# Kernel tuning notes

Hardware: AMD Instinct MI355X
Metric: run time of the kernel (lower is better)

The kernel has to match this reference:

```python
import jax, jax.numpy as jnp
import numpy as np

K = 3; STRIDE = 1; PAD = 1
IN_C = 256; OUT_C = 512
M = 5; TABLE_SIZE = 16
D = K * K * IN_C  # 2304


def _P(v, m):
    # ALSH preprocessing transform: append norm powers ||v||^2, ||v||^4, ...
    n2 = jnp.sum(v * v)
    powers = jnp.stack([n2 ** (2 ** i) for i in range(m)])
    return jnp.concatenate([v, powers])


def _Q(v, m):
    # ALSH query transform: append m halves
    return jnp.concatenate([v, jnp.full((m,), 0.5, v.dtype)])


def _hash_index(a, v):
    # hf followed by fmod(table_size).abs() as in the torch module
    h = jnp.floor(jnp.dot(a, v))
    return jnp.abs(jnp.mod(h, TABLE_SIZE)).astype(jnp.int32)


def _im2col(x):
    # x: (N, C, H, W) -> (K*K*C, N*h2*w2), rows ordered (kh, kw, c) to match
    # the (out, k, k, in) kernel flattening of the original module.
    N, C, H, W = x.shape
    h2 = (H - K + 2 * PAD) // STRIDE + 1
    w2 = (W - K + 2 * PAD) // STRIDE + 1
    xp = jnp.pad(x, ((0, 0), (0, 0), (PAD, PAD), (PAD, PAD)))
    cols = []
    for i in range(K):          # small fixed loop (k*k = 9)
        for j in range(K):
            cols.append(xp[:, :, i:i + h2 * STRIDE:STRIDE, j:j + w2 * STRIDE:STRIDE])
    p = jnp.stack(cols, 0)                 # (K*K, N, C, h2, w2)
    p = p.transpose(0, 2, 1, 3, 4)         # (K*K, C, N, h2, w2)
    return p.reshape(K * K * C, N * h2 * w2), h2, w2


def setup_inputs() -> dict:
    key = jax.random.key(0)
    k1, k2, k3, k4 = jax.random.split(key, 4)
    stdv = 1.0 / np.sqrt(IN_C * K * K)
    x = jax.random.normal(k1, (16, IN_C, 56, 56), dtype=jnp.float32)
    kernels = jax.random.uniform(k2, (OUT_C, D), dtype=jnp.float32,
                                 minval=-stdv, maxval=stdv)
    bias = jax.random.uniform(k3, (1, OUT_C, 1, 1), dtype=jnp.float32,
                              minval=-stdv, maxval=stdv)
    a = jax.random.normal(k4, (D + M,), dtype=jnp.float32)
    return {"x": x, "kernels": kernels, "bias": bias, "a": a, "mode": 0}


def reference(x, kernels, bias, a, mode):
    N = x.shape[0]
    patch_matr, h2, w2 = _im2col(x)  # (D, N*h2*w2)

    # --- build ALSH table: hash index per kernel row (non-differentiable) ---
    kernel_idx = jax.lax.stop_gradient(
        jax.vmap(lambda kr: _hash_index(a, _P(kr, M)))(kernels))  # (OUT_C,)

    # --- query: max over each patch row, normalized to unit vector ---
    max_row = patch_matr.max(axis=1)                    # (D,)
    unit = max_row / jnp.linalg.norm(max_row)
    q_idx = jax.lax.stop_gradient(_hash_index(a, _Q(unit, M)))

    # --- routed subset matmul, expressed as a row mask (jit-safe) ---
    mask = (kernel_idx == q_idx)                        # (OUT_C,) bool
    count = mask.sum()
    full = kernels @ patch_matr                         # (OUT_C, N*h2*w2)
    scale = jnp.where(count > 0, count / OUT_C, 1.0).astype(full.dtype)
    out = jnp.where(count > 0,
                    jnp.where(mask[:, None], full, 0.0) / scale,
                    full)

    out = out.reshape(OUT_C, N, h2 * w2).transpose(1, 0, 2)
    out = out.reshape(N, OUT_C, h2, w2)
    return out + bias
```

## Files before the change

kernel.cpp:

```cpp
#include <hip/hip_runtime.h>
#include <math.h>

#define IN_C   256
#define OUT_C  512
#define HW     3136
#define W_     56
#define D_     2304
#define TBL    16


#define XB_OFF 2375680ULL
#define XB_ROW 1856
#define P_OFF  7483392

typedef __attribute__((ext_vector_type(8))) __bf16 bf16x8;
typedef __attribute__((ext_vector_type(4))) float f32x4;

__device__ __forceinline__ ushort f2bf(float f) {
  uint b = __float_as_uint(f);
  b = b + 0x7FFFu + ((b >> 16) & 1u);
  return (ushort)(b >> 16);
}


__global__ __launch_bounds__(256) void k_setup(const float* __restrict__ x,
                                               const float* __restrict__ kern,
                                               const float* __restrict__ a,
                                               float* __restrict__ ws) {
  __shared__ __align__(16) float smem[64 * 57];
  int bx = blockIdx.x, t = threadIdx.x;

  if (bx < 3712) {
    int c0i = bx & 3;
    int n = (bx >> 2) & 15;
    int yp = bx >> 6;
    int c0 = c0i * 64, cgbase = c0i * 2;
    ushort* xb = (ushort*)((char*)ws + XB_OFF);
    const size_t CGS = (size_t)16 * 58 * XB_ROW;
    size_t rb0 = (size_t)(n * 58 + yp) * XB_ROW;
    uint4 z4 = make_uint4(0u, 0u, 0u, 0u);

    if (yp == 0 || yp == 57) {
      for (int e = t; e < 464; e += 256) {
        int cg_l = e / 232, k = e - cg_l * 232;
        *(uint4*)&xb[rb0 + (size_t)(cgbase + cg_l) * CGS + (size_t)k * 8] = z4;
      }
      return;
    }
    if (t < 16) {
      int cg_l = t >> 3, r = t & 7;
      int wp = (r >> 2) ? 57 : 0, oct = r & 3;
      *(uint4*)&xb[rb0 + (size_t)(cgbase + cg_l) * CGS + wp * 32 + oct * 8] = z4;
    }
    int y = yp - 1;
    float* Lf = smem;
    for (int e = t; e < 3584; e += 256) {
      int ci = e / 56, w = e - ci * 56;
      Lf[ci * 57 + w] = x[(size_t)(n * 256 + c0 + ci) * 3136 + y * 56 + w];
    }
    __syncthreads();
    for (int e = t; e < 448; e += 256) {
      int w = e >> 3, cg_l = (e >> 2) & 1, oct = e & 3;
      int cb = cg_l * 32 + oct * 8;
      uint pk[4];
#pragma unroll
      for (int k = 0; k < 4; k++) {
        uint lo = f2bf(Lf[(cb + 2 * k) * 57 + w]);
        uint hi = f2bf(Lf[(cb + 2 * k + 1) * 57 + w]);
        pk[k] = lo | (hi << 16);
      }
      *(uint4*)&xb[rb0 + (size_t)(cgbase + cg_l) * CGS + (w + 1) * 32 + oct * 8] =
          make_uint4(pk[0], pk[1], pk[2], pk[3]);
    }
  } else if (bx < 4736) {
    int idx = bx - 3712;
    int c = idx & 255, part = idx >> 8;
    float m[3][3];
#pragma unroll
    for (int i = 0; i < 3; i++)
#pragma unroll
      for (int j = 0; j < 3; j++) m[i][j] = -INFINITY;
    for (int e = t; e < 4 * HW; e += 256) {
      int nl = e / HW;
      int rem = e - nl * HW;
      int r = rem / W_;
      int s = rem - r * W_;
      float v = x[(size_t)((part * 4 + nl) * IN_C + c) * HW + rem];
      bool rc[3] = { r <= 54, true, r >= 1 };
      bool sc[3] = { s <= 54, true, s >= 1 };
#pragma unroll
      for (int i = 0; i < 3; i++)
#pragma unroll
        for (int j = 0; j < 3; j++)
          if (rc[i] && sc[j]) m[i][j] = fmaxf(m[i][j], v);
    }
#pragma unroll
    for (int i = 0; i < 3; i++)
#pragma unroll
      for (int j = 0; j < 3; j++)
        for (int o = 32; o; o >>= 1)
          m[i][j] = fmaxf(m[i][j], __shfl_down(m[i][j], o, 64));
    float* red = smem;
    int lane = t & 63, wid = t >> 6;
    if (lane == 0) {
#pragma unroll
      for (int i = 0; i < 3; i++)
#pragma unroll
        for (int j = 0; j < 3; j++) red[wid * 9 + i * 3 + j] = m[i][j];
    }
    __syncthreads();
    if (t < 9) {
      float v = fmaxf(fmaxf(red[0 * 9 + t], red[1 * 9 + t]),
                      fmaxf(red[2 * 9 + t], red[3 * 9 + t]));
      ws[P_OFF + (size_t)part * 2304 + (size_t)t * IN_C + c] = v;
    }
  } else if (bx < 5248) {
    int o = bx - 4736;
    const float* kr = kern + (size_t)o * D_;
    double sd = 0, sn = 0;
    for (int d = t; d < D_; d += 256) {
      double w = (double)kr[d];
      sd += (double)a[d] * w;
      sn += w * w;
    }
    double* sh = (double*)smem;
    double* sh2 = sh + 8;
    int lane = t & 63, wid = t >> 6;
    for (int off = 32; off; off >>= 1) {
      sd += __shfl_down(sd, off, 64);
      sn += __shfl_down(sn, off, 64);
    }
    if (lane == 0) { sh[wid] = sd; sh2[wid] = sn; }
    __syncthreads();
    if (t == 0) {
      double td = 0, tn = 0;
      for (int w = 0; w < 4; w++) { td += sh[w]; tn += sh2[w]; }
      double p1 = tn, p2 = p1 * p1, p4 = p2 * p2, p8 = p4 * p4, p16 = p8 * p8;
      td += (double)a[D_] * p1 + (double)a[D_ + 1] * p2 + (double)a[D_ + 2] * p4 +
            (double)a[D_ + 3] * p8 + (double)a[D_ + 4] * p16;
      long long h = (long long)floor(td);
      ((int*)ws)[2304 + o] = (int)((h % TBL + TBL) % TBL);
    }
  } else {
    int s = bx - 5248;
    uint* Wc = (uint*)((char*)ws + 16384);
    const float* src = kern + (size_t)s * D_;
    for (int e = t; e < 1152; e += 256) {
      uint lo = f2bf(src[2 * e]);
      uint hi = f2bf(src[2 * e + 1]);
      Wc[(size_t)s * 1152 + e] = lo | (hi << 16);
    }
  }
}

__global__ __launch_bounds__(512) void k_route(const float* __restrict__ a,
                                               float* __restrict__ ws) {
  int t = threadIdx.x;
  const float* P = ws + P_OFF;
  __shared__ double sh[8], sh2[8];
  __shared__ int shq, c1, c2;
  double sd = 0.0, sq = 0.0;
  if (t < 256) {
    for (int d = t; d < D_; d += 256) {
      float v = fmaxf(fmaxf(P[d], P[2304 + d]), fmaxf(P[4608 + d], P[6912 + d]));
      if ((d >> 8) != 4) v = fmaxf(v, 0.0f);
      double dv = (double)v;
      sd += (double)a[d] * dv;
      sq += dv * dv;
    }
    for (int o = 32; o; o >>= 1) {
      sd += __shfl_down(sd, o, 64);
      sq += __shfl_down(sq, o, 64);
    }
    if ((t & 63) == 0) { sh[t >> 6] = sd; sh2[t >> 6] = sq; }
  }
  __syncthreads();
  if (t == 0) {
    double td = 0, tq = 0;
    for (int w = 0; w < 4; w++) { td += sh[w]; tq += sh2[w]; }
    double dot = td / sqrt(tq);
    dot += 0.5 * ((double)a[D_] + (double)a[D_ + 1] + (double)a[D_ + 2] +
                  (double)a[D_ + 3] + (double)a[D_ + 4]);
    long long h = (long long)floor(dot);
    int q = (int)((h % TBL + TBL) % TBL);
    ((int*)ws)[2816] = q;
    shq = q;
    c1 = 0; c2 = 0;
  }
  __syncthreads();
  int* hashk = (int*)ws + 2304;
  int* cntp = (int*)ws + 2817;
  float* scalep = ws + 2818;
  int* active = (int*)ws + 2819;
  int* inact = (int*)ws + 3331;
  int q = shq;
  bool m = (hashk[t] == q);
  if (m) active[atomicAdd(&c1, 1)] = t;
  else   inact[atomicAdd(&c2, 1)] = t;
  __syncthreads();
  int c = c1;
  if (c == 0) active[t] = t;
  if (t == 0) {
    if (c > 0) { *cntp = c; *scalep = 512.0f / (float)c; }
    else       { *cntp = 512; *scalep = 1.0f; }
  }
}

#define XSTR 40
#define XSTRIDE 40
#define ASTRIDE 104

__global__ __launch_bounds__(256, 1) void k_convx(const float* __restrict__ bias,
                                                  const float* __restrict__ ws,
                                                  float* __restrict__ out) {
  const int* iws = (const int*)ws;
  int cnt = iws[2817];
  int octile = blockIdx.y;
  int rt = blockIdx.x;
  int n = blockIdx.z;
  int t = threadIdx.x;

  {
    int base = octile * 128;
    int lo = base < cnt ? cnt : base;
    int hi = base + 128;
    if (lo < hi) {
      const int* inact = iws + 3331;
      size_t nbase = (size_t)n * OUT_C * HW;
      int nin = hi - lo;
      for (int e = t; e < nin * 112; e += 256) {
        int j = e / 112, f = e - j * 112;
        int oc = inact[lo - cnt + j];
        float bv = bias[oc];
        ((float4*)out)[(nbase + (size_t)oc * HW) / 4 + rt * 112 + f] =
            make_float4(bv, bv, bv, bv);
      }
    }
    if (base >= cnt) return;
  }

  float sc = ws[2818];
  const int* active = iws + 2819;
  const char* Wcb = (const char*)ws + 16384;
  const ushort* xb = (const ushort*)((const char*)ws + XB_OFF);

  int lane = t & 63, wid = t >> 6;
  int quad = lane >> 4, l16 = lane & 15;

  __shared__ __align__(16) ushort X_lds[2][580 * XSTR];
  __shared__ __align__(16) ushort A_lds[2][128 * XSTR];

  int pbase[7];
#pragma unroll
  for (int b = 0; b < 7; b++) {
    int pxl = wid * 112 + b * 16 + l16;
    int rl = pxl / 56;
    int col = pxl - rl * 56;
    pbase[b] = ((rl + 1) * 58 + (col + 1)) * XSTR;
  }

  int r0 = t >> 2;
  int slot0 = octile * 128 + r0;
  int slot1 = slot0 + 64;
  int aoc0 = (slot0 < cnt) ? active[slot0] : 0;
  int aoc1 = (slot1 < cnt) ? active[slot1] : 0;
  const char* Wr0 = Wcb + (size_t)aoc0 * 4608 + (t & 3) * 16;
  const char* Wr1 = Wcb + (size_t)aoc1 * 4608 + (t & 3) * 16;
  int aoff0 = r0 * XSTR + (t & 3) * 8;
  int aoff1 = (r0 + 64) * XSTR + (t & 3) * 8;

  const size_t CGS = (size_t)16 * 58 * XB_ROW;
  const ushort* xsrc = xb + (size_t)(n * 58 + rt * 8) * XB_ROW;

  f32x4 acc[8][7];
#pragma unroll
  for (int a = 0; a < 8; a++)
#pragma unroll
    for (int b = 0; b < 7; b++) acc[a][b] = (f32x4){0.f, 0.f, 0.f, 0.f};

  uint4 xh0 = {}, xh1 = {};

  {
    uint4 a0 = *(const uint4*)Wr0;
    uint4 a1 = *(const uint4*)Wr1;
    *(uint4*)&A_lds[0][aoff0] = a0;
    *(uint4*)&A_lds[0][aoff1] = a1;
    for (int j = t; j < 2320; j += 256)
      *(uint4*)&X_lds[0][(j >> 2) * XSTR + (j & 3) * 8] =
          *(const uint4*)(xsrc + (size_t)j * 8);
  }
  __syncthreads();

  for (int cc = 0; cc < 8; ++cc) {
    const int xc = cc & 1;
#pragma unroll
    for (int tap = 0; tap < 9; ++tap) {
      const int cur = (cc + tap) & 1;
      const int tapn = (tap + 1) % 9;
      const int ccn = cc + (tap + 1) / 9;
      const bool havenext = !(cc == 7 && tap == 8);
      uint4 na0, na1;
      if (havenext) {
        int off = tapn * 512 + ccn * 64;
        na0 = *(const uint4*)(Wr0 + off);
        na1 = *(const uint4*)(Wr1 + off);
      }
      const bool xi = (tap < 8) && (cc < 7);
      uint4 xv0, xv1;
      if (xi) {
        int xj = tap * 290 + t;
        xv0 = *(const uint4*)(xsrc + (size_t)(cc + 1) * CGS + (size_t)xj * 8);
        if (t < 34)
          xv1 = *(const uint4*)(xsrc + (size_t)(cc + 1) * CGS +
                                (size_t)(xj + 256) * 8);
      }

      const int kh = tap / 3, kw = tap - kh * 3;
      const int poff = ((kh - 1) * 58 + (kw - 1)) * XSTR + quad * 8;
      bf16x8 xf[7];
#pragma unroll
      for (int b = 0; b < 7; b++) {
        union { uint4 u; bf16x8 v; } cv;
        cv.u = *(const uint4*)&X_lds[xc][pbase[b] + poff];
        xf[b] = cv.v;
      }
      __builtin_amdgcn_s_setprio(1);
#pragma unroll
      for (int a = 0; a < 8; a++) {
        union { uint4 u; bf16x8 v; } av;
        av.u = *(const uint4*)&A_lds[cur][(a * 16 + l16) * XSTR + quad * 8];
        bf16x8 af = av.v;
#pragma unroll
        for (int b = 0; b < 7; b++)
          acc[a][b] = __builtin_amdgcn_mfma_f32_16x16x32_bf16(af, xf[b],
                                                              acc[a][b], 0, 0, 0);
      }
      __builtin_amdgcn_s_setprio(0);

      if (havenext) {
        *(uint4*)&A_lds[cur ^ 1][aoff0] = na0;
        *(uint4*)&A_lds[cur ^ 1][aoff1] = na1;
      }
      if (tap >= 1 && cc < 7) {
        int hj = (tap - 1) * 290 + t;
        *(uint4*)&X_lds[xc ^ 1][(hj >> 2) * XSTR + (hj & 3) * 8] = xh0;
        if (t < 34) {
          int hj2 = hj + 256;
          *(uint4*)&X_lds[xc ^ 1][(hj2 >> 2) * XSTR + (hj2 & 3) * 8] = xh1;
        }
      }
      xh0 = xv0; xh1 = xv1;
      __syncthreads();
    }
  }

  size_t nbase = (size_t)n * OUT_C * HW;
#pragma unroll
  for (int a = 0; a < 8; a++) {
#pragma unroll
    for (int r = 0; r < 4; r++) {
      int slot = octile * 128 + a * 16 + quad * 4 + r;
      if (slot < cnt) {
        int oc = active[slot];
        float bv = bias[oc];
        size_t obase = nbase + (size_t)oc * HW + rt * 448 + wid * 112 + l16;
#pragma unroll
        for (int b = 0; b < 7; b++)
          out[obase + b * 16] = acc[a][b][r] * sc + bv;
      }
    }
  }
}


__global__ __launch_bounds__(256) void k_chanmax(const float* __restrict__ x,
                                                 float* __restrict__ ws) {
  int c = blockIdx.x, t = threadIdx.x;
  float m[3][3];
#pragma unroll
  for (int i = 0; i < 3; i++)
#pragma unroll
    for (int j = 0; j < 3; j++) m[i][j] = -INFINITY;
  for (int e = t; e < 16 * HW; e += 256) {
    int n = e / HW;
    int rem = e - n * HW;
    int r = rem / W_;
    int s = rem - r * W_;
    float v = x[(size_t)(n * IN_C + c) * HW + rem];
    bool rc[3] = { r <= 54, true, r >= 1 };
    bool sc[3] = { s <= 54, true, s >= 1 };
#pragma unroll
    for (int i = 0; i < 3; i++)
#pragma unroll
      for (int j = 0; j < 3; j++)
        if (rc[i] && sc[j]) m[i][j] = fmaxf(m[i][j], v);
  }
#pragma unroll
  for (int i = 0; i < 3; i++)
#pragma unroll
    for (int j = 0; j < 3; j++)
      for (int o = 32; o; o >>= 1)
        m[i][j] = fmaxf(m[i][j], __shfl_down(m[i][j], o, 64));
  __shared__ float red[4][9];
  int lane = t & 63, wid = t >> 6;
  if (lane == 0) {
#pragma unroll
    for (int i = 0; i < 3; i++)
#pragma unroll
      for (int j = 0; j < 3; j++) red[wid][i * 3 + j] = m[i][j];
  }
  __syncthreads();
  if (t < 9) {
    float v = fmaxf(fmaxf(red[0][t], red[1][t]), fmaxf(red[2][t], red[3][t]));
    int i = t / 3, j = t - i * 3;
    if (i != 1 || j != 1) v = fmaxf(v, 0.0f);
    ws[(size_t)t * IN_C + c] = v;
  }
}

__global__ __launch_bounds__(256) void k_qhash(const float* __restrict__ a,
                                               float* __restrict__ ws) {
  const float* max_row = ws;
  int t = threadIdx.x;
  double sd = 0.0, sq = 0.0;
  for (int d = t; d < D_; d += 256) {
    double v = (double)max_row[d];
    sd += (double)a[d] * v;
    sq += v * v;
  }
  __shared__ double sh[8], sh2[8];
  int lane = t & 63, wid = t >> 6;
  for (int o = 32; o; o >>= 1) {
    sd += __shfl_down(sd, o, 64);
    sq += __shfl_down(sq, o, 64);
  }
  if (lane == 0) { sh[wid] = sd; sh2[wid] = sq; }
  __syncthreads();
  if (t == 0) {
    double td = 0, tq = 0;
    for (int w = 0; w < 4; w++) { td += sh[w]; tq += sh2[w]; }
    double dot = td / sqrt(tq);
    dot += 0.5 * ((double)a[D_] + (double)a[D_ + 1] + (double)a[D_ + 2] +
                  (double)a[D_ + 3] + (double)a[D_ + 4]);
    long long h = (long long)floor(dot);
    ((int*)ws)[2816] = (int)((h % TBL + TBL) % TBL);
  }
}

__global__ __launch_bounds__(256) void k_khash(const float* __restrict__ kern,
                                               const float* __restrict__ a,
                                               float* __restrict__ ws) {
  int o = blockIdx.x, t = threadIdx.x;
  const float* kr = kern + (size_t)o * D_;
  double sd = 0, sn = 0;
  for (int d = t; d < D_; d += 256) {
    double w = (double)kr[d];
    sd += (double)a[d] * w;
    sn += w * w;
  }
  __shared__ double sh[8], sh2[8];
  int lane = t & 63, wid = t >> 6;
  for (int off = 32; off; off >>= 1) {
    sd += __shfl_down(sd, off, 64);
    sn += __shfl_down(sn, off, 64);
  }
  if (lane == 0) { sh[wid] = sd; sh2[wid] = sn; }
  __syncthreads();
  if (t == 0) {
    double td = 0, tn = 0;
    for (int w = 0; w < 4; w++) { td += sh[w]; tn += sh2[w]; }
    double p1 = tn, p2 = p1 * p1, p4 = p2 * p2, p8 = p4 * p4, p16 = p8 * p8;
    td += (double)a[D_] * p1 + (double)a[D_ + 1] * p2 + (double)a[D_ + 2] * p4 +
          (double)a[D_ + 3] * p8 + (double)a[D_ + 4] * p16;
    long long h = (long long)floor(td);
    ((int*)ws)[2304 + o] = (int)((h % TBL + TBL) % TBL);
  }
}

__global__ __launch_bounds__(512) void k_select(float* __restrict__ ws) {
  int t = threadIdx.x;
  int* hashk = (int*)ws + 2304;
  int* qidx = (int*)ws + 2816;
  int* cntp = (int*)ws + 2817;
  float* scalep = ws + 2818;
  int* active = (int*)ws + 2819;
  int* flags = (int*)ws + 3331;
  __shared__ int cnt;
  if (t == 0) cnt = 0;
  active[t] = 0;
  __syncthreads();
  int q = *qidx;
  bool m = (hashk[t] == q);
  if (m) {
    int p = atomicAdd(&cnt, 1);
    active[p] = t;
  }
  __syncthreads();
  int c = cnt;
  flags[t] = (c == 0) ? 1 : (m ? 1 : 0);
  if (c == 0) active[t] = t;
  if (t == 0) {
    if (c > 0) { *cntp = c; *scalep = 512.0f / (float)c; }
    else       { *cntp = 512; *scalep = 1.0f; }
  }
}

__global__ __launch_bounds__(256) void k_prep(const float* __restrict__ kern,
                                              float* __restrict__ ws) {
  const int* iws = (const int*)ws;
  int cnt = iws[2817];
  const int* active = iws + 2819;
  ushort* Wc = (ushort*)((char*)ws + 16384);
  int s = blockIdx.x, t = threadIdx.x;
  if (s < cnt) {
    int oc = active[s];
    const float* src = kern + (size_t)oc * D_;
    for (int e = t; e < D_; e += 256) Wc[(size_t)s * D_ + e] = f2bf(src[e]);
  } else {
    for (int e = t; e < D_; e += 256) Wc[(size_t)s * D_ + e] = 0;
  }
}

__global__ __launch_bounds__(256) void k_biasfill(const float* __restrict__ bias,
                                                  const float* __restrict__ ws,
                                                  float* __restrict__ out) {
  const int* flags = (const int*)ws + 3331;
  const int total4 = 16 * OUT_C * HW / 4;
  int stride = gridDim.x * blockDim.x;
  for (int i = blockIdx.x * blockDim.x + threadIdx.x; i < total4; i += stride) {
    int o = (i / 784) & (OUT_C - 1);
    if (!flags[o]) {
      float b = bias[o];
      ((float4*)out)[i] = make_float4(b, b, b, b);
    }
  }
}

__global__ __launch_bounds__(256, 2) void k_conv(const float* __restrict__ x,
                                                 const float* __restrict__ bias,
                                                 const float* __restrict__ ws,
                                                 float* __restrict__ out) {
  const int* iws = (const int*)ws;
  int cnt = iws[2817];
  int octile = blockIdx.y;
  if (octile * 128 >= cnt) return;
  float sc = ws[2818];
  const int* active = iws + 2819;
  const ushort* Wc = (const ushort*)((const char*)ws + 16384);
  int rt = blockIdx.x;
  int n = blockIdx.z;
  int t = threadIdx.x;
  int lane = t & 63, wid = t >> 6;
  int quad = lane >> 4, l16 = lane & 15;
  int ochalf = wid & 1, pxhalf = wid >> 1;
  __shared__ __align__(16) ushort X_lds[348 * XSTRIDE];
  __shared__ __align__(16) ushort A_lds[128 * ASTRIDE];
  const float* xin = x + (size_t)n * IN_C * HW;
  int pbase[7];
#pragma unroll
  for (int b = 0; b < 7; b++) {
    int pxl = pxhalf * 112 + b * 16 + l16;
    int rl = pxl / 56;
    int col = pxl - rl * 56;
    pbase[b] = ((rl + 1) * 58 + (col + 1)) * XSTRIDE;
  }
  f32x4 acc[4][7];
#pragma unroll
  for (int a = 0; a < 4; a++)
#pragma unroll
    for (int b = 0; b < 7; b++) acc[a][b] = (f32x4){0.f, 0.f, 0.f, 0.f};
  for (int cc = 0; cc < 8; ++cc) {
    int c0 = cc * 32;
    __syncthreads();
    for (int e = t; e < 1392; e += 256) {
      int q = e / 348;
      int p = e - q * 348;
      int rl = p / 58;
      int cp = p - rl * 58;
      int y = rt * 4 - 1 + rl;
      int xx = cp - 1;
      float vv[8];
      if ((unsigned)y < 56u && (unsigned)xx < 56u) {
        const float* src = xin + (size_t)(c0 + q * 8) * HW + y * W_ + xx;
#pragma unroll
        for (int k = 0; k < 8; k++) vv[k] = src[(size_t)k * HW];
      } else {
#pragma unroll
        for (int k = 0; k < 8; k++) vv[k] = 0.f;
      }
      uint4 pk;
      pk.x = (uint)f2bf(vv[0]) | ((uint)f2bf(vv[1]) << 16);
      pk.y = (uint)f2bf(vv[2]) | ((uint)f2bf(vv[3]) << 16);
      pk.z = (uint)f2bf(vv[4]) | ((uint)f2bf(vv[5]) << 16);
      pk.w = (uint)f2bf(vv[6]) | ((uint)f2bf(vv[7]) << 16);
      *(uint4*)&X_lds[p * XSTRIDE + q * 8] = pk;
    }
    for (int kh = 0; kh < 3; ++kh) {
      __syncthreads();
      for (int e = t; e < 1536; e += 256) {
        int oc = e / 12;
        int seg = e - oc * 12;
        int tl = seg >> 2, q = seg & 3;
        uint4 v = *(const uint4*)(Wc + (size_t)(octile * 128 + oc) * D_ +
                                  (kh * 3 + tl) * IN_C + c0 + q * 8);
        *(uint4*)&A_lds[oc * ASTRIDE + tl * 32 + q * 8] = v;
      }
      __syncthreads();
      int di = kh - 1;
#pragma unroll
      for (int djj = 0; djj < 3; ++djj) {
        int poff = (di * 58 + (djj - 1)) * XSTRIDE + quad * 8;
        bf16x8 bfr[7];
#pragma unroll
        for (int b = 0; b < 7; b++) {
          union { uint4 u; bf16x8 v; } cv;
          cv.u = *(const uint4*)&X_lds[pbase[b] + poff];
          bfr[b] = cv.v;
        }
#pragma unroll
        for (int a = 0; a < 4; a++) {
          union { uint4 u; bf16x8 v; } cv;
          cv.u = *(const uint4*)&A_lds[(ochalf * 64 + a * 16 + l16) * ASTRIDE +
                                       djj * 32 + quad * 8];
          bf16x8 af = cv.v;
#pragma unroll
          for (int b = 0; b < 7; b++)
            acc[a][b] = __builtin_amdgcn_mfma_f32_16x16x32_bf16(af, bfr[b],
                                                                acc[a][b], 0, 0, 0);
        }
      }
    }
  }
  size_t nbase = (size_t)n * OUT_C * HW;
#pragma unroll
  for (int a = 0; a < 4; a++) {
#pragma unroll
    for (int r = 0; r < 4; r++) {
      int slot = octile * 128 + ochalf * 64 + a * 16 + quad * 4 + r;
      if (slot < cnt) {
        int oc = active[slot];
        float bv = bias[oc];
        size_t obase = nbase + (size_t)oc * HW + rt * 224 + pxhalf * 112 + l16;
#pragma unroll
        for (int b = 0; b < 7; b++)
          out[obase + b * 16] = acc[a][b][r] * sc + bv;
      }
    }
  }
}

extern "C" void kernel_launch(void* const* d_in, const int* in_sizes, int n_in,
                              void* d_out, int out_size, void* d_ws, size_t ws_size,
                              hipStream_t stream) {
  const float* x    = (const float*)d_in[0];
  const float* kern = (const float*)d_in[1];
  const float* bias = (const float*)d_in[2];
  const float* a    = (const float*)d_in[3];
  float* out = (float*)d_out;
  float* ws  = (float*)d_ws;

  const size_t need = 29933568ULL + 4 * 2304 * 4;

  if (ws_size >= need) {
    k_setup<<<dim3(5760), dim3(256), 0, stream>>>(x, kern, a, ws);
    k_route<<<dim3(1), dim3(512), 0, stream>>>(a, ws);
    k_convx<<<dim3(7, 4, 16), dim3(256), 0, stream>>>(bias, ws, out);
  } else {
    k_chanmax<<<dim3(IN_C), dim3(256), 0, stream>>>(x, ws);
    k_qhash<<<dim3(1), dim3(256), 0, stream>>>(a, ws);
    k_khash<<<dim3(OUT_C), dim3(256), 0, stream>>>(kern, a, ws);
    k_select<<<dim3(1), dim3(512), 0, stream>>>(ws);
    k_prep<<<dim3(OUT_C), dim3(256), 0, stream>>>(kern, ws);
    k_biasfill<<<dim3(4096), dim3(256), 0, stream>>>(bias, ws, out);
    k_conv<<<dim3(14, 4, 16), dim3(256), 0, stream>>>(x, bias, ws, out);
  }
}
```

Before: 323.0 us.

## Double output-channel tile per block to 256 with 512-thread blocks sharing X tile

The conv kernel now uses 512-thread blocks covering 256 output channels, where before it used 256 threads and 128 channels. Two wave groups split the channel range and share one staged input-patch tile in LDS. This halves the number of blocks and the redundant X loads across channel tiles, and spreads X staging over more threads. The costs are a larger LDS footprint, fewer blocks (224) on a large-CU GPU, and more idle work when few channels are active, since whole 256-channel tiles compute even when the count is small.

```diff
diff --git a/kernel.cpp b/kernel.cpp
--- a/kernel.cpp
+++ b/kernel.cpp
@@ -210,7 +210,7 @@
 #define XSTRIDE 40
 #define ASTRIDE 104
 
-__global__ __launch_bounds__(256, 1) void k_convx(const float* __restrict__ bias,
+__global__ __launch_bounds__(512, 2) void k_convx(const float* __restrict__ bias,
                                                   const float* __restrict__ ws,
                                                   float* __restrict__ out) {
   const int* iws = (const int*)ws;
@@ -221,14 +221,14 @@
   int t = threadIdx.x;
 
   {
-    int base = octile * 128;
+    int base = octile * 256;
     int lo = base < cnt ? cnt : base;
-    int hi = base + 128;
+    int hi = base + 256;
     if (lo < hi) {
       const int* inact = iws + 3331;
       size_t nbase = (size_t)n * OUT_C * HW;
       int nin = hi - lo;
-      for (int e = t; e < nin * 112; e += 256) {
+      for (int e = t; e < nin * 112; e += 512) {
         int j = e / 112, f = e - j * 112;
         int oc = inact[lo - cnt + j];
         float bv = bias[oc];
@@ -246,28 +246,31 @@
 
   int lane = t & 63, wid = t >> 6;
   int quad = lane >> 4, l16 = lane & 15;
+  int ochalf = wid >> 2;
+  int pxq = wid & 3;
 
   __shared__ __align__(16) ushort X_lds[2][580 * XSTR];
-  __shared__ __align__(16) ushort A_lds[2][128 * XSTR];
+  __shared__ __align__(16) ushort A_lds[2][256 * XSTR];
 
   int pbase[7];
 #pragma unroll
   for (int b = 0; b < 7; b++) {
-    int pxl = wid * 112 + b * 16 + l16;
+    int pxl = pxq * 112 + b * 16 + l16;
     int rl = pxl / 56;
     int col = pxl - rl * 56;
     pbase[b] = ((rl + 1) * 58 + (col + 1)) * XSTR;
   }
 
   int r0 = t >> 2;
-  int slot0 = octile * 128 + r0;
-  int slot1 = slot0 + 64;
+  int q = t & 3;
+  int slot0 = octile * 256 + r0;
+  int slot1 = slot0 + 128;
   int aoc0 = (slot0 < cnt) ? active[slot0] : 0;
   int aoc1 = (slot1 < cnt) ? active[slot1] : 0;
-  const char* Wr0 = Wcb + (size_t)aoc0 * 4608 + (t & 3) * 16;
-  const char* Wr1 = Wcb + (size_t)aoc1 * 4608 + (t & 3) * 16;
-  int aoff0 = r0 * XSTR + (t & 3) * 8;
-  int aoff1 = (r0 + 64) * XSTR + (t & 3) * 8;
+  const char* Wr0 = Wcb + (size_t)aoc0 * 4608 + q * 16;
+  const char* Wr1 = Wcb + (size_t)aoc1 * 4608 + q * 16;
+  int aoff0 = r0 * XSTR + q * 8;
+  int aoff1 = (r0 + 128) * XSTR + q * 8;
 
   const size_t CGS = (size_t)16 * 58 * XB_ROW;
   const ushort* xsrc = xb + (size_t)(n * 58 + rt * 8) * XB_ROW;
@@ -278,14 +281,14 @@
 #pragma unroll
     for (int b = 0; b < 7; b++) acc[a][b] = (f32x4){0.f, 0.f, 0.f, 0.f};
 
-  uint4 xh0 = {}, xh1 = {};
+  uint4 xh0 = {};
 
   {
     uint4 a0 = *(const uint4*)Wr0;
     uint4 a1 = *(const uint4*)Wr1;
     *(uint4*)&A_lds[0][aoff0] = a0;
     *(uint4*)&A_lds[0][aoff1] = a1;
-    for (int j = t; j < 2320; j += 256)
+    for (int j = t; j < 2320; j += 512)
       *(uint4*)&X_lds[0][(j >> 2) * XSTR + (j & 3) * 8] =
           *(const uint4*)(xsrc + (size_t)j * 8);
   }
@@ -305,14 +308,11 @@
         na0 = *(const uint4*)(Wr0 + off);
         na1 = *(const uint4*)(Wr1 + off);
       }
-      const bool xi = (tap < 8) && (cc < 7);
-      uint4 xv0, xv1;
+      const bool xi = (tap < 8) && (cc < 7) && (t < 290);
+      uint4 xv0;
       if (xi) {
         int xj = tap * 290 + t;
         xv0 = *(const uint4*)(xsrc + (size_t)(cc + 1) * CGS + (size_t)xj * 8);
-        if (t < 34)
-          xv1 = *(const uint4*)(xsrc + (size_t)(cc + 1) * CGS +
-                                (size_t)(xj + 256) * 8);
       }
 
       const int kh = tap / 3, kw = tap - kh * 3;
@@ -328,7 +328,8 @@
 #pragma unroll
       for (int a = 0; a < 8; a++) {
         union { uint4 u; bf16x8 v; } av;
-        av.u = *(const uint4*)&A_lds[cur][(a * 16 + l16) * XSTR + quad * 8];
+        av.u = *(const uint4*)&A_lds[cur][(ochalf * 128 + a * 16 + l16) * XSTR +
+                                          quad * 8];
         bf16x8 af = av.v;
 #pragma unroll
         for (int b = 0; b < 7; b++)
@@ -341,15 +342,11 @@
         *(uint4*)&A_lds[cur ^ 1][aoff0] = na0;
         *(uint4*)&A_lds[cur ^ 1][aoff1] = na1;
       }
-      if (tap >= 1 && cc < 7) {
+      if (tap >= 1 && cc < 7 && t < 290) {
         int hj = (tap - 1) * 290 + t;
         *(uint4*)&X_lds[xc ^ 1][(hj >> 2) * XSTR + (hj & 3) * 8] = xh0;
-        if (t < 34) {
-          int hj2 = hj + 256;
-          *(uint4*)&X_lds[xc ^ 1][(hj2 >> 2) * XSTR + (hj2 & 3) * 8] = xh1;
-        }
-      }
-      xh0 = xv0; xh1 = xv1;
+      }
+      xh0 = xv0;
       __syncthreads();
     }
   }
@@ -359,11 +356,11 @@
   for (int a = 0; a < 8; a++) {
 #pragma unroll
     for (int r = 0; r < 4; r++) {
-      int slot = octile * 128 + a * 16 + quad * 4 + r;
+      int slot = octile * 256 + ochalf * 128 + a * 16 + quad * 4 + r;
       if (slot < cnt) {
         int oc = active[slot];
         float bv = bias[oc];
-        size_t obase = nbase + (size_t)oc * HW + rt * 448 + wid * 112 + l16;
+        size_t obase = nbase + (size_t)oc * HW + rt * 448 + pxq * 112 + l16;
 #pragma unroll
         for (int b = 0; b < 7; b++)
           out[obase + b * 16] = acc[a][b][r] * sc + bv;
@@ -664,7 +661,7 @@
   if (ws_size >= need) {
     k_setup<<<dim3(5760), dim3(256), 0, stream>>>(x, kern, a, ws);
     k_route<<<dim3(1), dim3(512), 0, stream>>>(a, ws);
-    k_convx<<<dim3(7, 4, 16), dim3(256), 0, stream>>>(bias, ws, out);
+    k_convx<<<dim3(7, 2, 16), dim3(512), 0, stream>>>(bias, ws, out);
   } else {
     k_chanmax<<<dim3(IN_C), dim3(256), 0, stream>>>(x, ws);
     k_qhash<<<dim3(1), dim3(256), 0, stream>>>(a, ws);
```

Result: slower. 881.0 us (+172.7%).
